# Optimization experiments

Hardware: AMD Instinct MI355X
Metric: run time of the kernel (lower is better)

Reference implementation:

```python
import math
import jax, jax.numpy as jnp
import numpy as np

B, T, D_MODEL, H = 8, 2048, 1024, 16
D_HEAD = D_MODEL // H


def _rel_shift(x):
    # x: (B, T, H, H) -- faithful port of the TF pad/reshape/slice trick,
    # which in this module operates on the time axis (dim 1).
    b, t, h, h2 = x.shape
    x = jnp.pad(x, ((0, 0), (1, 0), (0, 0), (0, 0)))  # (B, T+1, H, H)
    x = x.reshape(t + 1, b, h, h2)[1:]                 # drop first row
    return x.reshape(b, t, h, h2)


def setup_inputs() -> dict:
    key = jax.random.key(0)
    ks = jax.random.split(key, 16)
    s = 1.0 / math.sqrt(D_MODEL)
    return {
        "inputs": jax.random.normal(ks[0], (B, T, D_MODEL), jnp.float32),
        "pos_embedding": jax.random.normal(ks[1], (B, T, D_MODEL), jnp.float32),
        "masks": jnp.ones((B, T), dtype=bool),
        "Wq": jax.random.normal(ks[2], (D_MODEL, D_MODEL), jnp.float32) * s,
        "bq": jnp.zeros((D_MODEL,), jnp.float32),
        "Wk": jax.random.normal(ks[3], (D_MODEL, D_MODEL), jnp.float32) * s,
        "bk": jnp.zeros((D_MODEL,), jnp.float32),
        "Wv": jax.random.normal(ks[4], (D_MODEL, D_MODEL), jnp.float32) * s,
        "bv": jnp.zeros((D_MODEL,), jnp.float32),
        "Wp": jax.random.normal(ks[5], (D_MODEL, D_MODEL), jnp.float32) * s,
        "Wo": jax.random.normal(ks[6], (D_MODEL, D_MODEL), jnp.float32) * s,
        "bo": jnp.zeros((D_MODEL,), jnp.float32),
        "u_bias": jax.random.normal(ks[7], (H, D_HEAD), jnp.float32) * 0.05,
        "v_bias": jax.random.normal(ks[8], (H, D_HEAD), jnp.float32) * 0.05,
    }


def reference(inputs, pos_embedding, masks, Wq, bq, Wk, bk, Wv, bv, Wp, Wo, bo, u_bias, v_bias):
    b, t, _ = inputs.shape
    sqrt_dim = math.sqrt(D_MODEL)
    q = (inputs @ Wq + bq).reshape(b, t, H, D_HEAD)
    k = (inputs @ Wk + bk).reshape(b, t, H, D_HEAD)
    v = (inputs @ Wv + bv).reshape(b, t, H, D_HEAD)
    p = (pos_embedding @ Wp).reshape(b, t, H, D_HEAD)

    # NOTE: no (B,H,T,D) transpose in the original -> HxH scores per timestep.
    content_score = jnp.einsum("bthd,btkd->bthk", q + u_bias, k)  # (B,T,H,H)
    pos_score = jnp.einsum("bthd,btkd->bthk", q + v_bias, p)      # (B,T,H,H)
    pos_score = _rel_shift(pos_score)
    score = (content_score + pos_score) / sqrt_dim
    score = jnp.where(masks[:, :, None, None], score, jnp.float32(1e-9))
    attn = jax.nn.softmax(score, axis=-1)
    ctx = jnp.einsum("bthk,btkd->bthd", attn, v)                  # (B,T,H,D)
    ctx = ctx.transpose(0, 2, 1, 3).reshape(b, -1, D_MODEL)       # (B,T,d_model)
    return ctx @ Wo + bo
```

## Files before the change

### kernel.cpp

```cpp
#include <hip/hip_runtime.h>


typedef __attribute__((ext_vector_type(8))) short short8;
typedef __attribute__((ext_vector_type(4))) float f32x4;

__device__ __forceinline__ ushort f2bf(float f) {
    unsigned u = __float_as_uint(f);
    u += 0x7FFFu + ((u >> 16) & 1u);
    return (ushort)(u >> 16);
}
__device__ __forceinline__ float bf2f(ushort u) {
    return __uint_as_float(((unsigned)u) << 16);
}

typedef const unsigned int __attribute__((address_space(1)))* gas_t;
typedef unsigned int __attribute__((address_space(3)))* las_t;
__device__ __forceinline__ void gl_lds16(const ushort* g, ushort* l) {
    __builtin_amdgcn_global_load_lds((gas_t)g, (las_t)l, 16, 0, 0);
}

__global__ __launch_bounds__(256)
void conv_bf16_k(const float* __restrict__ in, ushort* __restrict__ out)
{
    const size_t i = ((size_t)blockIdx.x * 256 + threadIdx.x) * 8;
    float4 a = *(const float4*)(in + i);
    float4 b = *(const float4*)(in + i + 4);
    short8 o = {(short)f2bf(a.x), (short)f2bf(a.y), (short)f2bf(a.z), (short)f2bf(a.w),
                (short)f2bf(b.x), (short)f2bf(b.y), (short)f2bf(b.z), (short)f2bf(b.w)};
    *(short8*)(out + i) = o;
}

__global__ __launch_bounds__(256)
void transpose_convert_k(const float* __restrict__ W, ushort* __restrict__ Wt, int K, int N)
{
    __shared__ float tile[32][33];
    const int tx = threadIdx.x & 31;
    const int ty = threadIdx.x >> 5;
    const int n0 = blockIdx.x * 32;
    const int k0 = blockIdx.y * 32;
#pragma unroll
    for (int i = 0; i < 4; ++i)
        tile[ty + i * 8][tx] = W[(size_t)(k0 + ty + i * 8) * N + n0 + tx];
    __syncthreads();
#pragma unroll
    for (int i = 0; i < 4; ++i)
        Wt[(size_t)(n0 + ty + i * 8) * K + k0 + tx] = f2bf(tile[tx][ty + i * 8]);
}

__global__ __launch_bounds__(256)
void bias_concat_k(const float* __restrict__ b0, const float* __restrict__ b1,
                   const float* __restrict__ b2, float* __restrict__ out)
{
    const int i = blockIdx.x * 256 + threadIdx.x;
    const int s = i >> 10;
    const int j = i & 1023;
    out[i] = (s == 0) ? b0[j] : (s == 1) ? b1[j] : b2[j];
}


#define VMC(n) asm volatile("s_waitcnt vmcnt(" #n ")" ::: "memory")

#define STAGE_A(tt, ss) do { \
    ushort* hh = AsF + ((((tt)&1)*2 + (ss)) * 8192) + lchunk; \
    const ushort* gg = Ag + (size_t)(tt) * 64 + (ss) * 32; \
    gl_lds16(gg, hh); \
    gl_lds16(gg + row128, hh + 4096); \
} while (0)

#define STAGE_B(tt, ss) do { \
    ushort* hh = BsF + ((((tt)&1)*2 + (ss)) * 8192) + lchunk; \
    const ushort* gg = Bg + (size_t)(tt) * 64 + (ss) * 32; \
    gl_lds16(gg, hh); \
    gl_lds16(gg + row128, hh + 4096); \
} while (0)

#define PHASE2(dd, ss, STAGE_STMT, VM_STMT) do { \
    const ushort* ap = AsF + ((dd)*2 + (ss)) * 8192 + (wr*128 + lr) * 32 + fb; \
    const ushort* bp = BsF + ((dd)*2 + (ss)) * 8192 + (wc*64 + lr) * 32 + fb; \
    short8 af[8], bfr[4]; \
    _Pragma("unroll") \
    for (int i_ = 0; i_ < 8; ++i_) af[i_] = *(const short8*)(ap + i_ * 512); \
    _Pragma("unroll") \
    for (int i_ = 0; i_ < 4; ++i_) bfr[i_] = *(const short8*)(bp + i_ * 512); \
    STAGE_STMT; \
    __builtin_amdgcn_s_barrier(); \
    __builtin_amdgcn_sched_barrier(0); \
    __builtin_amdgcn_s_setprio(1); \
    _Pragma("unroll") \
    for (int i_ = 0; i_ < 8; ++i_) \
        _Pragma("unroll") \
        for (int n_ = 0; n_ < 4; ++n_) \
            acc[i_][n_] = __builtin_amdgcn_mfma_f32_16x16x32_bf16(af[i_], bfr[n_], acc[i_][n_], 0, 0, 0); \
    __builtin_amdgcn_s_setprio(0); \
    __builtin_amdgcn_sched_barrier(0); \
    VM_STMT; \
    __builtin_amdgcn_s_barrier(); \
    __builtin_amdgcn_sched_barrier(0); \
} while (0)

template<int HAS_BIAS, int OUT_BF16>
__global__ __launch_bounds__(512, 2)
void gemm4_k(const ushort* __restrict__ A, const ushort* __restrict__ Bt,
             const float* __restrict__ bias, void* __restrict__ Cv,
             int N, int K)
{
    __shared__ ushort AsF[32768];
    __shared__ ushort BsF[32768];
    const int tid = threadIdx.x;
    const int l = tid & 63;
    const int w = tid >> 6;
    const int wr = w >> 2;
    const int wc = w & 3;

    const int gx = gridDim.x;
    const int lin = blockIdx.y * gx + blockIdx.x;
    const int xcd = lin & 7;
    const int idx = lin >> 3;
    const int hb = gridDim.y >> 3;
    const int sxc = gx >> 2;
    const int g4 = idx >> 4;
    const int li = idx & 15;
    const int bx = (g4 % sxc) * 4 + (li & 3);
    const int by = xcd * hb + (g4 / sxc) * 4 + (li >> 2);
    const int bm = by * 256;
    const int bn = bx * 256;
    const int NT = K >> 6;

    const int srow = w * 16 + (l >> 2);
    const int scol = ((l & 3) ^ ((l >> 3) & 3)) * 8;
    const ushort* Ag = A  + (size_t)(bm + srow) * K + scol;
    const ushort* Bg = Bt + (size_t)(bn + srow) * K + scol;
    const size_t row128 = (size_t)128 * K;
    const int lchunk = w * 512;

    const int lr = l & 15;
    const int fb = (((l >> 4) ^ ((l >> 1) & 3)) * 8);

    f32x4 acc[8][4];
#pragma unroll
    for (int i = 0; i < 8; ++i)
#pragma unroll
        for (int n = 0; n < 4; ++n)
            acc[i][n] = (f32x4){0.f, 0.f, 0.f, 0.f};

    STAGE_A(0, 0); STAGE_B(0, 0);
    STAGE_A(0, 1); STAGE_B(0, 1);
    STAGE_A(1, 0); STAGE_B(1, 0);
    VMC(8);
    __builtin_amdgcn_s_barrier();
    __builtin_amdgcn_sched_barrier(0);

    for (int t = 0; t < NT; ++t) {
        const int d = t & 1;
        PHASE2(d, 0, { if (t + 1 < NT) { STAGE_A(t + 1, 1); STAGE_B(t + 1, 1); } },
               { if (t == NT - 1) VMC(0); else VMC(8); });
        PHASE2(d, 1, { if (t + 2 < NT) { STAGE_A(t + 2, 0); STAGE_B(t + 2, 0); } },
               { if (t == NT - 2) VMC(4); else if (t == NT - 1) VMC(0); else VMC(8); });
    }

    const int cr = (l >> 4) * 4;
    const int cc = l & 15;
    float bv[4];
#pragma unroll
    for (int n = 0; n < 4; ++n)
        bv[n] = HAS_BIAS ? bias[bn + wc * 64 + n * 16 + cc] : 0.f;
#pragma unroll
    for (int m = 0; m < 8; ++m) {
#pragma unroll
        for (int n = 0; n < 4; ++n) {
            const int col = bn + wc * 64 + n * 16 + cc;
#pragma unroll
            for (int r = 0; r < 4; ++r) {
                const int row = bm + wr * 128 + m * 16 + cr + r;
                float v = acc[m][n][r] + bv[n];
                if (OUT_BF16) ((ushort*)Cv)[(size_t)row * N + col] = f2bf(v);
                else          ((float*)Cv)[(size_t)row * N + col] = v;
            }
        }
    }
}

__global__ __launch_bounds__(256)
void attn_k(const ushort* __restrict__ qkv, const ushort* __restrict__ pbuf,
            const float* __restrict__ ubias, const float* __restrict__ vbias,
            const int* __restrict__ masks, ushort* __restrict__ ctx)
{
    __shared__ float qu[16][65];
    __shared__ float kk[16][65];
    __shared__ float vv[16][65];
    __shared__ float qv[16][65];
    __shared__ float pp[16][65];
    __shared__ float at[16][16];

    const int m  = blockIdx.x;
    const int b2 = m >> 11;
    const int t2 = m & 2047;
    const int f  = m + 8;
    const int bs = f / 2049;
    const int ts = f - bs * 2049;
    const bool haspos = (ts != 0);
    const int mp = bs * 2048 + ts - 1;

    const int tid = threadIdx.x;
    const int e = tid * 4;
    const int h = e >> 6;
    const int d = e & 63;

    {
        const ushort* base = qkv + (size_t)m * 3072;
        ushort4 a = *(const ushort4*)(base + e);
        ushort4 b = *(const ushort4*)(base + 1024 + e);
        ushort4 c = *(const ushort4*)(base + 2048 + e);
        float4 uu = *(const float4*)(ubias + e);
        qu[h][d + 0] = bf2f(a.x) + uu.x;
        qu[h][d + 1] = bf2f(a.y) + uu.y;
        qu[h][d + 2] = bf2f(a.z) + uu.z;
        qu[h][d + 3] = bf2f(a.w) + uu.w;
        kk[h][d + 0] = bf2f(b.x);
        kk[h][d + 1] = bf2f(b.y);
        kk[h][d + 2] = bf2f(b.z);
        kk[h][d + 3] = bf2f(b.w);
        vv[h][d + 0] = bf2f(c.x);
        vv[h][d + 1] = bf2f(c.y);
        vv[h][d + 2] = bf2f(c.z);
        vv[h][d + 3] = bf2f(c.w);
        if (haspos) {
            ushort4 qq = *(const ushort4*)(qkv + (size_t)mp * 3072 + e);
            ushort4 pq = *(const ushort4*)(pbuf + (size_t)mp * 1024 + e);
            float4 vv4 = *(const float4*)(vbias + e);
            qv[h][d + 0] = bf2f(qq.x) + vv4.x;
            qv[h][d + 1] = bf2f(qq.y) + vv4.y;
            qv[h][d + 2] = bf2f(qq.z) + vv4.z;
            qv[h][d + 3] = bf2f(qq.w) + vv4.w;
            pp[h][d + 0] = bf2f(pq.x);
            pp[h][d + 1] = bf2f(pq.y);
            pp[h][d + 2] = bf2f(pq.z);
            pp[h][d + 3] = bf2f(pq.w);
        } else {
            qv[h][d + 0] = 0.f; qv[h][d + 1] = 0.f; qv[h][d + 2] = 0.f; qv[h][d + 3] = 0.f;
            pp[h][d + 0] = 0.f; pp[h][d + 1] = 0.f; pp[h][d + 2] = 0.f; pp[h][d + 3] = 0.f;
        }
    }
    __syncthreads();

    const int sh = tid >> 4;
    const int sk = tid & 15;
    float cs = 0.f, ps = 0.f;
#pragma unroll 8
    for (int dd = 0; dd < 64; ++dd) {
        cs += qu[sh][dd] * kk[sk][dd];
        ps += qv[sh][dd] * pp[sk][dd];
    }
    float score = (cs + ps) * 0.03125f;
    score = (masks[m] != 0) ? score : 1e-9f;

    float mx = score;
#pragma unroll
    for (int o = 8; o; o >>= 1) mx = fmaxf(mx, __shfl_xor(mx, o, 64));
    float ex = __expf(score - mx);
    float sum = ex;
#pragma unroll
    for (int o = 8; o; o >>= 1) sum += __shfl_xor(sum, o, 64);
    at[sh][sk] = ex / sum;
    __syncthreads();

#pragma unroll
    for (int j = 0; j < 4; ++j) {
        const int idx = tid + j * 256;
        const int hh = idx >> 6;
        const int dd2 = idx & 63;
        float s = 0.f;
#pragma unroll
        for (int k2 = 0; k2 < 16; ++k2)
            s += at[hh][k2] * vv[k2][dd2];
        const size_t orow = (size_t)b2 * 2048 + hh * 128 + (t2 >> 4);
        ctx[orow * 1024 + (t2 & 15) * 64 + dd2] = f2bf(s);
    }
}

extern "C" void kernel_launch(void* const* d_in, const int* in_sizes, int n_in,
                              void* d_out, int out_size, void* d_ws, size_t ws_size,
                              hipStream_t stream)
{
    (void)in_sizes; (void)n_in; (void)out_size; (void)ws_size;
    const float* inputs = (const float*)d_in[0];
    const float* pos    = (const float*)d_in[1];
    const int*   masks  = (const int*)d_in[2];
    const float* Wq = (const float*)d_in[3];
    const float* bq = (const float*)d_in[4];
    const float* Wk = (const float*)d_in[5];
    const float* bk = (const float*)d_in[6];
    const float* Wv = (const float*)d_in[7];
    const float* bv = (const float*)d_in[8];
    const float* Wp = (const float*)d_in[9];
    const float* Wo = (const float*)d_in[10];
    const float* bo = (const float*)d_in[11];
    const float* ub = (const float*)d_in[12];
    const float* vb = (const float*)d_in[13];

    char* ws = (char*)d_ws;
    const size_t WT_SZ = (size_t)1024 * 1024 * 2;
    ushort* WqT = (ushort*)(ws);
    ushort* WkT = (ushort*)(ws + 1 * WT_SZ);
    ushort* WvT = (ushort*)(ws + 2 * WT_SZ);
    ushort* WpT = (ushort*)(ws + 3 * WT_SZ);
    ushort* WoT = (ushort*)(ws + 4 * WT_SZ);
    float*  biascat = (float*)(ws + 5 * WT_SZ);
    char* bufs = ws + 5 * WT_SZ + 65536;
    const size_t S_SZ = (size_t)16384 * 1024 * 2;
    ushort* S1 = (ushort*)(bufs);
    ushort* S2 = (ushort*)(bufs + S_SZ);
    ushort* S3 = (ushort*)(bufs + 2 * S_SZ);

    dim3 blk(256);
    dim3 tgrid(32, 32);

    transpose_convert_k<<<tgrid, blk, 0, stream>>>(Wq, WqT, 1024, 1024);
    transpose_convert_k<<<tgrid, blk, 0, stream>>>(Wk, WkT, 1024, 1024);
    transpose_convert_k<<<tgrid, blk, 0, stream>>>(Wv, WvT, 1024, 1024);
    transpose_convert_k<<<tgrid, blk, 0, stream>>>(Wp, WpT, 1024, 1024);
    transpose_convert_k<<<tgrid, blk, 0, stream>>>(Wo, WoT, 1024, 1024);
    bias_concat_k<<<dim3(12), blk, 0, stream>>>(bq, bk, bv, biascat);

    conv_bf16_k<<<dim3(8192), blk, 0, stream>>>(pos, S1);
    gemm4_k<0, 1><<<dim3(4, 64), dim3(512), 0, stream>>>(S1, WpT, nullptr, S2, 1024, 1024);

    conv_bf16_k<<<dim3(8192), blk, 0, stream>>>(inputs, S1);
    gemm4_k<1, 1><<<dim3(12, 64), dim3(512), 0, stream>>>(S1, WqT, biascat, S3, 3072, 1024);

    attn_k<<<dim3(16384), blk, 0, stream>>>(S3, S2, ub, vb, masks, S1);

    gemm4_k<1, 0><<<dim3(4, 64), dim3(512), 0, stream>>>(S1, WoT, bo, (float*)d_out, 1024, 1024);
}
```

Before: 331.9 us.

## Split GEMM main loop into four finer phases with per-phase A/B staging

Restructures the bf16 GEMM pipeline so each 32-wide K sub-slice is processed in two half-M phases, with B fragments reused across halves. Global-to-LDS staging is now issued one operand at a time per phase and prefetches only one tile ahead instead of a deeper schedule. The aim is smaller register footprint per phase and finer interleaving of loads with MFMA, at the cost of more barriers per K-step and reduced prefetch depth.

```diff
diff --git a/kernel.cpp b/kernel.cpp
--- a/kernel.cpp
+++ b/kernel.cpp
@@ -74,23 +74,26 @@
     gl_lds16(gg + row128, hh + 4096); \
 } while (0)
 
-#define PHASE2(dd, ss, STAGE_STMT, VM_STMT) do { \
-    const ushort* ap = AsF + ((dd)*2 + (ss)) * 8192 + (wr*128 + lr) * 32 + fb; \
-    const ushort* bp = BsF + ((dd)*2 + (ss)) * 8192 + (wc*64 + lr) * 32 + fb; \
-    short8 af[8], bfr[4]; \
+#define PHASE5(dd, ss, mh, READ_B, STAGE_STMT, VM_STMT) do { \
+    const ushort* ap = AsF + ((dd)*2 + (ss)) * 8192 + (wr*128 + (mh)*64 + lr) * 32 + fb; \
+    short8 af[4]; \
     _Pragma("unroll") \
-    for (int i_ = 0; i_ < 8; ++i_) af[i_] = *(const short8*)(ap + i_ * 512); \
-    _Pragma("unroll") \
-    for (int i_ = 0; i_ < 4; ++i_) bfr[i_] = *(const short8*)(bp + i_ * 512); \
+    for (int i_ = 0; i_ < 4; ++i_) af[i_] = *(const short8*)(ap + i_ * 512); \
+    if (READ_B) { \
+        const ushort* bp = BsF + ((dd)*2 + (ss)) * 8192 + (wc*64 + lr) * 32 + fb; \
+        _Pragma("unroll") \
+        for (int n_ = 0; n_ < 4; ++n_) bfr[n_] = *(const short8*)(bp + n_ * 512); \
+    } \
     STAGE_STMT; \
     __builtin_amdgcn_s_barrier(); \
+    asm volatile("s_waitcnt lgkmcnt(0)" ::: "memory"); \
     __builtin_amdgcn_sched_barrier(0); \
     __builtin_amdgcn_s_setprio(1); \
     _Pragma("unroll") \
-    for (int i_ = 0; i_ < 8; ++i_) \
+    for (int i_ = 0; i_ < 4; ++i_) \
         _Pragma("unroll") \
         for (int n_ = 0; n_ < 4; ++n_) \
-            acc[i_][n_] = __builtin_amdgcn_mfma_f32_16x16x32_bf16(af[i_], bfr[n_], acc[i_][n_], 0, 0, 0); \
+            acc[(mh)*4 + i_][n_] = __builtin_amdgcn_mfma_f32_16x16x32_bf16(af[i_], bfr[n_], acc[(mh)*4 + i_][n_], 0, 0, 0); \
     __builtin_amdgcn_s_setprio(0); \
     __builtin_amdgcn_sched_barrier(0); \
     VM_STMT; \
@@ -100,7 +103,7 @@
 
 template<int HAS_BIAS, int OUT_BF16>
 __global__ __launch_bounds__(512, 2)
-void gemm4_k(const ushort* __restrict__ A, const ushort* __restrict__ Bt,
+void gemm5_k(const ushort* __restrict__ A, const ushort* __restrict__ Bt,
              const float* __restrict__ bias, void* __restrict__ Cv,
              int N, int K)
 {
@@ -142,20 +145,22 @@
 #pragma unroll
         for (int n = 0; n < 4; ++n)
             acc[i][n] = (f32x4){0.f, 0.f, 0.f, 0.f};
+    short8 bfr[4];
 
     STAGE_A(0, 0); STAGE_B(0, 0);
     STAGE_A(0, 1); STAGE_B(0, 1);
-    STAGE_A(1, 0); STAGE_B(1, 0);
-    VMC(8);
+    VMC(4);
     __builtin_amdgcn_s_barrier();
     __builtin_amdgcn_sched_barrier(0);
 
     for (int t = 0; t < NT; ++t) {
         const int d = t & 1;
-        PHASE2(d, 0, { if (t + 1 < NT) { STAGE_A(t + 1, 1); STAGE_B(t + 1, 1); } },
-               { if (t == NT - 1) VMC(0); else VMC(8); });
-        PHASE2(d, 1, { if (t + 2 < NT) { STAGE_A(t + 2, 0); STAGE_B(t + 2, 0); } },
-               { if (t == NT - 2) VMC(4); else if (t == NT - 1) VMC(0); else VMC(8); });
+        PHASE5(d, 0, 0, 1, { if (t + 1 < NT) STAGE_A(t + 1, 0); }, {});
+        PHASE5(d, 0, 1, 0, { if (t + 1 < NT) STAGE_B(t + 1, 0); },
+               { if (t == NT - 1) VMC(0); else VMC(4); });
+        PHASE5(d, 1, 0, 1, { if (t + 1 < NT) STAGE_A(t + 1, 1); }, {});
+        PHASE5(d, 1, 1, 0, { if (t + 1 < NT) STAGE_B(t + 1, 1); },
+               { if (t != NT - 1) VMC(4); });
     }
 
     const int cr = (l >> 4) * 4;
@@ -323,12 +328,12 @@
     bias_concat_k<<<dim3(12), blk, 0, stream>>>(bq, bk, bv, biascat);
 
     conv_bf16_k<<<dim3(8192), blk, 0, stream>>>(pos, S1);
-    gemm4_k<0, 1><<<dim3(4, 64), dim3(512), 0, stream>>>(S1, WpT, nullptr, S2, 1024, 1024);
+    gemm5_k<0, 1><<<dim3(4, 64), dim3(512), 0, stream>>>(S1, WpT, nullptr, S2, 1024, 1024);
 
     conv_bf16_k<<<dim3(8192), blk, 0, stream>>>(inputs, S1);
-    gemm4_k<1, 1><<<dim3(12, 64), dim3(512), 0, stream>>>(S1, WqT, biascat, S3, 3072, 1024);
+    gemm5_k<1, 1><<<dim3(12, 64), dim3(512), 0, stream>>>(S1, WqT, biascat, S3, 3072, 1024);
 
     attn_k<<<dim3(16384), blk, 0, stream>>>(S3, S2, ub, vb, masks, S1);
 
-    gemm4_k<1, 0><<<dim3(4, 64), dim3(512), 0, stream>>>(S1, WoT, bo, (float*)d_out, 1024, 1024);
-}
+    gemm5_k<1, 0><<<dim3(4, 64), dim3(512), 0, stream>>>(S1, WoT, bo, (float*)d_out, 1024, 1024);
+}
```

After: 328.7 us. Within noise of the previous version (-1.0%).

## Shrink GEMM tile to 128x256 with triple-buffered K=32 LDS pipeline

Applied to the files above, without the earlier changes.

Replaces the 256x256-tile GEMM, which used double buffering with two 32-wide K sub-stages, with a 128x256 tile that steps K by 32 through a three-slot LDS ring buffer. Each step has one barrier and prefetches two steps ahead. The smaller tile halves the accumulator registers and LDS use, so the launch bounds allow 4 blocks per CU and the grids double. The cost is less operand reuse per tile (more global and LDS traffic per FLOP) and more barriers per unit of K.

```diff
diff --git a/kernel.cpp b/kernel.cpp
--- a/kernel.cpp
+++ b/kernel.cpp
@@ -60,52 +60,14 @@
 
 #define VMC(n) asm volatile("s_waitcnt vmcnt(" #n ")" ::: "memory")
 
-#define STAGE_A(tt, ss) do { \
-    ushort* hh = AsF + ((((tt)&1)*2 + (ss)) * 8192) + lchunk; \
-    const ushort* gg = Ag + (size_t)(tt) * 64 + (ss) * 32; \
-    gl_lds16(gg, hh); \
-    gl_lds16(gg + row128, hh + 4096); \
-} while (0)
-
-#define STAGE_B(tt, ss) do { \
-    ushort* hh = BsF + ((((tt)&1)*2 + (ss)) * 8192) + lchunk; \
-    const ushort* gg = Bg + (size_t)(tt) * 64 + (ss) * 32; \
-    gl_lds16(gg, hh); \
-    gl_lds16(gg + row128, hh + 4096); \
-} while (0)
-
-#define PHASE2(dd, ss, STAGE_STMT, VM_STMT) do { \
-    const ushort* ap = AsF + ((dd)*2 + (ss)) * 8192 + (wr*128 + lr) * 32 + fb; \
-    const ushort* bp = BsF + ((dd)*2 + (ss)) * 8192 + (wc*64 + lr) * 32 + fb; \
-    short8 af[8], bfr[4]; \
-    _Pragma("unroll") \
-    for (int i_ = 0; i_ < 8; ++i_) af[i_] = *(const short8*)(ap + i_ * 512); \
-    _Pragma("unroll") \
-    for (int i_ = 0; i_ < 4; ++i_) bfr[i_] = *(const short8*)(bp + i_ * 512); \
-    STAGE_STMT; \
-    __builtin_amdgcn_s_barrier(); \
-    __builtin_amdgcn_sched_barrier(0); \
-    __builtin_amdgcn_s_setprio(1); \
-    _Pragma("unroll") \
-    for (int i_ = 0; i_ < 8; ++i_) \
-        _Pragma("unroll") \
-        for (int n_ = 0; n_ < 4; ++n_) \
-            acc[i_][n_] = __builtin_amdgcn_mfma_f32_16x16x32_bf16(af[i_], bfr[n_], acc[i_][n_], 0, 0, 0); \
-    __builtin_amdgcn_s_setprio(0); \
-    __builtin_amdgcn_sched_barrier(0); \
-    VM_STMT; \
-    __builtin_amdgcn_s_barrier(); \
-    __builtin_amdgcn_sched_barrier(0); \
-} while (0)
-
 template<int HAS_BIAS, int OUT_BF16>
-__global__ __launch_bounds__(512, 2)
-void gemm4_k(const ushort* __restrict__ A, const ushort* __restrict__ Bt,
+__global__ __launch_bounds__(512, 4)
+void gemm6_k(const ushort* __restrict__ A, const ushort* __restrict__ Bt,
              const float* __restrict__ bias, void* __restrict__ Cv,
              int N, int K)
 {
-    __shared__ ushort AsF[32768];
-    __shared__ ushort BsF[32768];
+    __shared__ ushort As[3 * 4096];
+    __shared__ ushort Bs[3 * 8192];
     const int tid = threadIdx.x;
     const int l = tid & 63;
     const int w = tid >> 6;
@@ -122,41 +84,74 @@
     const int li = idx & 15;
     const int bx = (g4 % sxc) * 4 + (li & 3);
     const int by = xcd * hb + (g4 / sxc) * 4 + (li >> 2);
-    const int bm = by * 256;
+    const int bm = by * 128;
     const int bn = bx * 256;
-    const int NT = K >> 6;
-
-    const int srow = w * 16 + (l >> 2);
-    const int scol = ((l & 3) ^ ((l >> 3) & 3)) * 8;
-    const ushort* Ag = A  + (size_t)(bm + srow) * K + scol;
-    const ushort* Bg = Bt + (size_t)(bn + srow) * K + scol;
-    const size_t row128 = (size_t)128 * K;
-    const int lchunk = w * 512;
+    const int NT = K >> 5;
+
+    const int srow = tid >> 2;
+    const int scol = ((tid & 3) ^ ((tid >> 3) & 3)) * 8;
+    const ushort* Ag  = A  + (size_t)(bm + srow) * K + scol;
+    const ushort* Bg  = Bt + (size_t)(bn + srow) * K + scol;
+    const ushort* Bg2 = Bg + (size_t)128 * K;
+    const int lw = w * 512;
 
     const int lr = l & 15;
     const int fb = (((l >> 4) ^ ((l >> 1) & 3)) * 8);
-
-    f32x4 acc[8][4];
-#pragma unroll
-    for (int i = 0; i < 8; ++i)
+    const int laneA = (wr * 64 + lr) * 32 + fb;
+    const int laneB = (wc * 64 + lr) * 32 + fb;
+
+    f32x4 acc[4][4];
+#pragma unroll
+    for (int i = 0; i < 4; ++i)
 #pragma unroll
         for (int n = 0; n < 4; ++n)
             acc[i][n] = (f32x4){0.f, 0.f, 0.f, 0.f};
 
-    STAGE_A(0, 0); STAGE_B(0, 0);
-    STAGE_A(0, 1); STAGE_B(0, 1);
-    STAGE_A(1, 0); STAGE_B(1, 0);
-    VMC(8);
+#define STAGE6(tt, rg) do { \
+    ushort* ha = As + (rg) * 4096 + lw; \
+    ushort* hb = Bs + (rg) * 8192 + lw; \
+    const size_t ko = (size_t)(tt) * 32; \
+    gl_lds16(Ag + ko, ha); \
+    gl_lds16(Bg + ko, hb); \
+    gl_lds16(Bg2 + ko, hb + 4096); \
+} while (0)
+
+    STAGE6(0, 0);
+    STAGE6(1, 1);
+    VMC(3);
     __builtin_amdgcn_s_barrier();
     __builtin_amdgcn_sched_barrier(0);
 
+    int cur = 0, stg = 2;
     for (int t = 0; t < NT; ++t) {
-        const int d = t & 1;
-        PHASE2(d, 0, { if (t + 1 < NT) { STAGE_A(t + 1, 1); STAGE_B(t + 1, 1); } },
-               { if (t == NT - 1) VMC(0); else VMC(8); });
-        PHASE2(d, 1, { if (t + 2 < NT) { STAGE_A(t + 2, 0); STAGE_B(t + 2, 0); } },
-               { if (t == NT - 2) VMC(4); else if (t == NT - 1) VMC(0); else VMC(8); });
-    }
+        if (t + 2 < NT) STAGE6(t + 2, stg);
+        const ushort* ap = As + cur * 4096 + laneA;
+        const ushort* bp = Bs + cur * 8192 + laneB;
+        short8 af[4], bf4[4];
+#pragma unroll
+        for (int m = 0; m < 4; ++m) af[m] = *(const short8*)(ap + m * 512);
+#pragma unroll
+        for (int n = 0; n < 4; ++n) bf4[n] = *(const short8*)(bp + n * 512);
+        asm volatile("s_waitcnt lgkmcnt(0)" ::: "memory");
+        __builtin_amdgcn_sched_barrier(0);
+        __builtin_amdgcn_s_setprio(1);
+#pragma unroll
+        for (int m = 0; m < 4; ++m)
+#pragma unroll
+            for (int n = 0; n < 4; ++n)
+                acc[m][n] = __builtin_amdgcn_mfma_f32_16x16x32_bf16(af[m], bf4[n], acc[m][n], 0, 0, 0);
+        __builtin_amdgcn_s_setprio(0);
+        __builtin_amdgcn_sched_barrier(0);
+        if (t < NT - 2) { VMC(3); }
+        else if (t == NT - 2) { VMC(0); }
+        if (t < NT - 1) {
+            __builtin_amdgcn_s_barrier();
+            __builtin_amdgcn_sched_barrier(0);
+        }
+        cur = (cur == 2) ? 0 : cur + 1;
+        stg = (stg == 2) ? 0 : stg + 1;
+    }
+#undef STAGE6
 
     const int cr = (l >> 4) * 4;
     const int cc = l & 15;
@@ -165,13 +160,13 @@
     for (int n = 0; n < 4; ++n)
         bv[n] = HAS_BIAS ? bias[bn + wc * 64 + n * 16 + cc] : 0.f;
 #pragma unroll
-    for (int m = 0; m < 8; ++m) {
+    for (int m = 0; m < 4; ++m) {
 #pragma unroll
         for (int n = 0; n < 4; ++n) {
             const int col = bn + wc * 64 + n * 16 + cc;
 #pragma unroll
             for (int r = 0; r < 4; ++r) {
-                const int row = bm + wr * 128 + m * 16 + cr + r;
+                const int row = bm + wr * 64 + m * 16 + cr + r;
                 float v = acc[m][n][r] + bv[n];
                 if (OUT_BF16) ((ushort*)Cv)[(size_t)row * N + col] = f2bf(v);
                 else          ((float*)Cv)[(size_t)row * N + col] = v;
@@ -323,12 +318,12 @@
     bias_concat_k<<<dim3(12), blk, 0, stream>>>(bq, bk, bv, biascat);
 
     conv_bf16_k<<<dim3(8192), blk, 0, stream>>>(pos, S1);
-    gemm4_k<0, 1><<<dim3(4, 64), dim3(512), 0, stream>>>(S1, WpT, nullptr, S2, 1024, 1024);
+    gemm6_k<0, 1><<<dim3(4, 128), dim3(512), 0, stream>>>(S1, WpT, nullptr, S2, 1024, 1024);
 
     conv_bf16_k<<<dim3(8192), blk, 0, stream>>>(inputs, S1);
-    gemm4_k<1, 1><<<dim3(12, 64), dim3(512), 0, stream>>>(S1, WqT, biascat, S3, 3072, 1024);
+    gemm6_k<1, 1><<<dim3(12, 128), dim3(512), 0, stream>>>(S1, WqT, biascat, S3, 3072, 1024);
 
     attn_k<<<dim3(16384), blk, 0, stream>>>(S3, S2, ub, vb, masks, S1);
 
-    gemm4_k<1, 0><<<dim3(4, 64), dim3(512), 0, stream>>>(S1, WoT, bo, (float*)d_out, 1024, 1024);
-}
+    gemm6_k<1, 0><<<dim3(4, 128), dim3(512), 0, stream>>>(S1, WoT, bo, (float*)d_out, 1024, 1024);
+}
```

Result: slower. 340.2 us (+2.5%).
